# Kernel tuning notes

Hardware: AMD Instinct MI355X
Metric: run time of the kernel (lower is better)

## Reference

```python
import jax, jax.numpy as jnp
import numpy as np

NC = 80
REG_MAX = 16
STRIDES = (8.0, 16.0, 32.0)
MAX_DET = 300
IOU_THR = 0.7
CONF_THR = 0.001
NCAND = 1024        # top candidates kept before greedy NMS
MAX_WH = 7680.0     # per-class offset trick (ultralytics max_wh)


def _make_anchors(shapes, strides, offset=0.5):
    pts, strs = [], []
    for (h, w), s in zip(shapes, strides):
        sx = jnp.arange(w, dtype=jnp.float32) + offset
        sy = jnp.arange(h, dtype=jnp.float32) + offset
        gy, gx = jnp.meshgrid(sy, sx, indexing='ij')
        pts.append(jnp.stack((gx, gy), -1).reshape(-1, 2))   # (h*w, 2)
        strs.append(jnp.full((h * w, 1), s, jnp.float32))
    return jnp.concatenate(pts, 0), jnp.concatenate(strs, 0)


def _decode_raw(feats):
    """feats_to_raw_yolov8: DFL decode + anchor transform -> pixel cxcywh + sigmoid cls."""
    B = feats[0].shape[0]
    no = 4 * REG_MAX + NC
    merged = jnp.concatenate([f.reshape(B, no, -1) for f in feats], axis=2)  # (B,no,A)
    dist, cls = merged[:, :4 * REG_MAX], merged[:, 4 * REG_MAX:]
    pd = dist.transpose(0, 2, 1).reshape(B, -1, 4, REG_MAX)                  # (B,A,4,reg_max)
    proj = jnp.arange(REG_MAX, dtype=merged.dtype)
    ltrb = jnp.einsum('bafr,r->baf', jax.nn.softmax(pd, -1), proj)           # (B,A,4)
    anchors, strd = _make_anchors([f.shape[2:] for f in feats], STRIDES)     # (A,2),(A,1)
    lt, rb = ltrb[..., :2], ltrb[..., 2:]
    x1y1 = anchors[None] - lt
    x2y2 = anchors[None] + rb
    cxy = (x1y1 + x2y2) * 0.5
    wh = x2y2 - x1y1
    dbox = jnp.concatenate((cxy, wh), -1) * strd[None]                       # (B,A,4) pixel cxcywh
    return dbox, jax.nn.sigmoid(cls).transpose(0, 2, 1)                      # (B,A,nc)


def _iou_one_vs_many(box, boxes):
    lt = jnp.maximum(box[:2], boxes[:, :2])
    rb = jnp.minimum(box[2:], boxes[:, 2:])
    inter = jnp.prod(jnp.clip(rb - lt, 0.0), -1)
    a1 = jnp.prod(box[2:] - box[:2])
    a2 = jnp.prod(boxes[:, 2:] - boxes[:, :2], -1)
    return inter / (a1 + a2 - inter + 1e-7)


def _nms_image(boxes_cxcywh, scores_cls):
    """conf threshold + per-class greedy NMS + max_det truncation -> (max_det, 6)."""
    conf = scores_cls.max(-1)                                   # (A,)
    cls = jnp.argmax(scores_cls, -1).astype(jnp.float32)        # (A,)
    conf = jnp.where(conf > CONF_THR, conf, 0.0)
    top_conf, idx = jax.lax.top_k(conf, NCAND)                  # candidate pre-selection
    cb = boxes_cxcywh[idx]                                      # (NCAND,4) cxcywh
    ccls = cls[idx]
    xy1 = cb[:, :2] - cb[:, 2:] * 0.5
    xy2 = cb[:, :2] + cb[:, 2:] * 0.5
    bx = jnp.concatenate((xy1, xy2), -1) + (ccls * MAX_WH)[:, None]  # class-offset xyxy

    def step(sc, _):
        j = jnp.argmax(sc)
        s = sc[j]
        sup = _iou_one_vs_many(bx[j], bx) > IOU_THR  # self-IoU=1 kills j as well
        return jnp.where(sup, 0.0, sc), (j, s)

    _, (sel, ss) = jax.lax.scan(step, top_conf, None, length=MAX_DET)
    rows = jnp.concatenate((cb[sel], ss[:, None], ccls[sel][:, None]), -1)  # (max_det,6)
    return jnp.where((ss > CONF_THR)[:, None], rows, 0.0)


def setup_inputs() -> dict:
    key = jax.random.key(0)
    k0, k1, k2 = jax.random.split(key, 3)
    B, no = 32, 4 * REG_MAX + NC
    return {
        'feat0': jax.random.normal(k0, (B, no, 80, 80), jnp.float32),
        'feat1': jax.random.normal(k1, (B, no, 40, 40), jnp.float32),
        'feat2': jax.random.normal(k2, (B, no, 20, 20), jnp.float32),
    }


def reference(feat0, feat1, feat2):
    dbox, ps = _decode_raw([feat0, feat1, feat2])        # (B,A,4), (B,A,nc)
    return jax.vmap(_nms_image)(dbox, ps)                # (B, max_det, 6)
```

## Files before the change

kernel.cpp:

```cpp
#include <hip/hip_runtime.h>
#include <stdint.h>

#define NCLS    80
#define NA_TOT  8400
#define NBATCH  32
#define MAXDET  300
#define SSORT   2048
#define RANKCAP 1536
#define CONFTHR 0.001f
#define TILES_PER_IMG 132

__device__ __forceinline__ float xla_expf(float in) {
  const float exp_hi = 88.3762626647950f;
  const float exp_lo = -88.3762626647949f;
  const float LOG2EF = 1.44269504088896341f;
  const float C1 = 0.693359375f;
  const float C2 = -2.12194440e-4f;
  const float p0 = 1.9875691500E-4f, p1 = 1.3981999507E-3f, p2 = 8.3334519073E-3f;
  const float p3 = 4.1665795894E-2f, p4 = 1.6666665459E-1f, p5 = 5.0000001201E-1f;
  float x = fminf(fmaxf(in, exp_lo), exp_hi);
  float fx = floorf(__fadd_rn(__fmul_rn(x, LOG2EF), 0.5f));
  float tmp = __fmul_rn(C1, fx);
  float z   = __fmul_rn(C2, fx);
  x = __fsub_rn(x, tmp);
  x = __fsub_rn(x, z);
  float y = __fadd_rn(__fmul_rn(x, p0), p1);
  y = __fadd_rn(__fmul_rn(y, x), p2);
  y = __fadd_rn(__fmul_rn(y, x), p3);
  y = __fadd_rn(__fmul_rn(y, x), p4);
  y = __fadd_rn(__fmul_rn(y, x), p5);
  y = __fadd_rn(__fmul_rn(y, __fmul_rn(x, x)), x);
  y = __fadd_rn(1.0f, y);
  int m = (int)fx;
  float s = __uint_as_float((uint32_t)(m + 127) << 23);
  float r = __fmul_rn(y, s);
  return fmaxf(r, in);
}

__device__ __forceinline__ float xla_sigmoid(float v) {
  float e = xla_expf(-v);
  float den = __fadd_rn(1.0f, e);
  return 1.0f / den;
}

__device__ __forceinline__ void gload_lds16(const float* gp, float* lp) {
  __builtin_amdgcn_global_load_lds(
      (const __attribute__((address_space(1))) void*)gp,
      (__attribute__((address_space(3))) void*)lp, 16, 0, 0);
}

__global__ __launch_bounds__(256) void yolo_decode_kernel(
    const float* __restrict__ f0, const float* __restrict__ f1,
    const float* __restrict__ f2,
    float4* __restrict__ oboxes, float* __restrict__ oconf,
    float* __restrict__ oclsf) {
  __shared__ float sm[4 * 144 * 16];
  int bx  = blockIdx.x;
  int b   = bx / TILES_PER_IMG;
  int r   = bx - b * TILES_PER_IMG;
  int tid = threadIdx.x;
  int lane = tid & 63;
  int wv   = tid >> 6;

  const float* base; int Alvl, W, a0, lvlbase; float stridef;
  if (r < 100)      { base = f0 + (size_t)b * (144 * 6400); W = 80; Alvl = 6400;
                      a0 = r * 64; stridef = 8.0f; lvlbase = 0; }
  else if (r < 125) { base = f1 + (size_t)b * (144 * 1600); W = 40; Alvl = 1600;
                      a0 = (r - 100) * 64; stridef = 16.0f; lvlbase = 6400; }
  else              { base = f2 + (size_t)b * (144 * 400);  W = 20; Alvl = 400;
                      int aa = (r - 125) * 64; a0 = (aa + 64 <= 400) ? aa : 336;
                      stridef = 32.0f; lvlbase = 8000; }

  int a0w = a0 + wv * 16;
  float* Sw = sm + wv * (144 * 16);

  #pragma unroll
  for (int k = 0; k < 9; ++k) {
    int ch = k * 16 + (lane >> 2);
    const float* gp = base + (size_t)ch * Alvl + a0w + (lane & 3) * 4;
    gload_lds16(gp, Sw + k * 256);
  }
  asm volatile("s_waitcnt vmcnt(0)" ::: "memory");
  __builtin_amdgcn_sched_barrier(0);

  int idx = lane & 15;
  int w   = lane >> 4;
  int ai  = a0w + idx;
  float ax = __fadd_rn((float)(ai % W), 0.5f);
  float ay = __fadd_rn((float)(ai / W), 0.5f);

  float d[16];
  float mx = -INFINITY;
  #pragma unroll
  for (int rr = 0; rr < 16; ++rr) {
    d[rr] = Sw[(w * 16 + rr) * 16 + idx];
    mx = fmaxf(mx, d[rr]);
  }
  float e[16]; float ssum = 0.0f;
  #pragma unroll
  for (int rr = 0; rr < 16; ++rr) {
    e[rr] = xla_expf(__fsub_rn(d[rr], mx));
    ssum = __fadd_rn(ssum, e[rr]);
  }
  float acc = 0.0f;
  #pragma unroll
  for (int rr = 0; rr < 16; ++rr) {
    float p = e[rr] / ssum;
    acc = __fadd_rn(acc, __fmul_rn(p, (float)rr));
  }

  float lt0 = __shfl(acc, idx + 0);
  float lt1 = __shfl(acc, idx + 16);
  float lt2 = __shfl(acc, idx + 32);
  float lt3 = __shfl(acc, idx + 48);

  float best = -INFINITY, second = -INFINITY; int bi = 0;
  #pragma unroll 5
  for (int kk = 0; kk < 20; ++kk) {
    int c = 64 + w * 20 + kk;
    float v = Sw[c * 16 + idx];
    if (v > best)        { second = best; best = v; bi = w * 20 + kk; }
    else if (v > second) { second = v; }
  }
  float gb = __shfl(best, idx + 0), gs = __shfl(second, idx + 0);
  int   gi = __shfl(bi,   idx + 0);
  #pragma unroll
  for (int qq = 1; qq < 4; ++qq) {
    float bq = __shfl(best, idx + qq * 16), sq = __shfl(second, idx + qq * 16);
    int   iq = __shfl(bi,   idx + qq * 16);
    if (bq > gb) { gs = fmaxf(gb, sq); gb = bq; gi = iq; }
    else         { gs = fmaxf(gs, bq); }
  }

  float conf = 0.0f; int cls = gi;
  if (__fsub_rn(gb, gs) < 1e-4f || gb > 5.0f) {
    if (w == 0) {
      float bs = -INFINITY; int bj = 0;
      for (int kk = 0; kk < NCLS; ++kk) {
        float v = Sw[(64 + kk) * 16 + idx];
        float s2 = xla_sigmoid(v);
        if (s2 > bs) { bs = s2; bj = kk; }
      }
      conf = bs; cls = bj;
    }
  } else {
    conf = xla_sigmoid(gb);
  }

  if (w == 0) {
    float x1 = __fsub_rn(ax, lt0);
    float y1 = __fsub_rn(ay, lt1);
    float x2 = __fadd_rn(ax, lt2);
    float y2 = __fadd_rn(ay, lt3);
    float cx = __fmul_rn(__fadd_rn(x1, x2), 0.5f);
    float cy = __fmul_rn(__fadd_rn(y1, y2), 0.5f);
    float ww = __fsub_rn(x2, x1);
    float hh = __fsub_rn(y2, y1);
    int t = b * NA_TOT + lvlbase + a0w + idx;
    oboxes[t] = make_float4(__fmul_rn(cx, stridef), __fmul_rn(cy, stridef),
                            __fmul_rn(ww, stridef), __fmul_rn(hh, stridef));
    conf = (conf > CONFTHR) ? conf : 0.0f;
    oconf[t] = conf;
    oclsf[t] = (float)cls;
  }
}

struct __align__(16) K2Lds {
  unsigned long long sortkeys[SSORT];
  unsigned confL[NA_TOT];
  unsigned hist[16][257];
  unsigned tot[257];
  unsigned Tarr[257];
};

__global__ __launch_bounds__(1024) void yolo_select_kernel(
    const float4* __restrict__ boxes, const float* __restrict__ conf,
    const float* __restrict__ clsf,
    float* __restrict__ g_rowd, unsigned long long* __restrict__ g_clsMask) {
  __shared__ K2Lds u;
  __shared__ unsigned s_need, s_prefix, s_found, s_B, s_scnt, s_cut, s_done;
  int b    = blockIdx.x;
  int tid  = threadIdx.x;
  int lane = tid & 63;
  int wv   = tid >> 6;
  const unsigned* confu = (const unsigned*)conf + (size_t)b * NA_TOT;
  float* rowd = g_rowd + (size_t)b * 1024 * 8;
  unsigned long long* cm = g_clsMask + (size_t)b * (NCLS * 16);

  for (int i = tid; i < NA_TOT; i += 1024) u.confL[i] = confu[i];
  {
    float4 z4 = make_float4(0.f, 0.f, 0.f, 0.f);
    float4* gr = (float4*)rowd;
    for (int k = tid; k < 2048; k += 1024) gr[k] = z4;
  }
  for (int i = tid; i < NCLS * 16; i += 1024) cm[i] = 0ull;
  if (tid == 0) { s_need = 1024; s_prefix = 0; s_cut = 0; s_done = 0; s_scnt = 0; }
  __syncthreads();

  for (int lv = 0; lv < 4; ++lv) {
    __syncthreads();
    if (s_done) break;
    for (int i = tid; i < 16 * 257; i += 1024) ((unsigned*)u.hist)[i] = 0;
    if (tid == 0) { s_found = 0; s_B = 0; }
    __syncthreads();
    unsigned pfx = s_prefix;
    for (int it = 0; it < 9; ++it) {
      int i = tid + it * 1024;
      unsigned c = (i < NA_TOT) ? u.confL[i] : 0u;
      bool in; unsigned bin;
      if (lv == 0)      { in = true;                bin = c >> 23; }
      else if (lv == 1) { in = ((c >> 23) == pfx);  bin = (c >> 15) & 0xFF; }
      else if (lv == 2) { in = ((c >> 15) == pfx);  bin = (c >> 7) & 0xFF; }
      else              { in = ((c >> 7)  == pfx);  bin = c & 0x7F; }
      bool act = (c != 0) && in;
      unsigned long long ab = __ballot(act);
      if (ab) {
        int fl = __ffsll(ab) - 1;
        unsigned fbin = __shfl(bin, fl);
        unsigned long long same = __ballot(act && (bin == fbin));
        if (same == ab) {
          if (lane == fl) atomicAdd(&u.hist[wv][fbin], (unsigned)__popcll(ab));
        } else if (act) {
          atomicAdd(&u.hist[wv][bin], 1u);
        }
      }
    }
    __syncthreads();
    if (tid < 256) {
      unsigned s = 0;
      #pragma unroll
      for (int q = 0; q < 16; ++q) s += u.hist[q][tid];
      u.tot[tid] = s;
    }
    __syncthreads();
    if (tid < 64) {
      unsigned carry = 0;
      if (tid == 0) u.Tarr[256] = 0;
      for (int ch = 3; ch >= 0; --ch) {
        int bb = ch * 64 + tid;
        unsigned v = u.tot[bb];
        #pragma unroll
        for (int off = 1; off < 64; off <<= 1) {
          unsigned t2 = __shfl_down(v, off);
          if (tid + off < 64) v += t2;
        }
        u.Tarr[bb] = v + carry;
        carry += __shfl(v, 0);
      }
    }
    __syncthreads();
    unsigned need = s_need;
    if (tid < 256) {
      unsigned h = u.tot[tid];
      if (h > 0 && u.Tarr[tid + 1] < need && u.Tarr[tid + 1] + h >= need) {
        s_B = (unsigned)tid; s_found = 1;
      }
    }
    __syncthreads();
    if (tid == 0) {
      if (!s_found) { s_cut = 1; s_done = 1; }
      else {
        unsigned B = s_B;
        unsigned selcnt = (1024u - need) + u.Tarr[B];
        if (selcnt <= (unsigned)RANKCAP || lv == 3) {
          s_done = 1;
          if (lv == 0)      s_cut = B << 23;
          else if (lv == 1) s_cut = (s_prefix << 23) | (B << 15);
          else if (lv == 2) s_cut = (s_prefix << 15) | (B << 7);
          else              s_cut = (s_prefix << 7)  | B;
        } else {
          s_need   = need - u.Tarr[B + 1];
          s_prefix = (s_prefix << 8) | B;
        }
      }
    }
  }
  __syncthreads();

  unsigned cut = s_cut;
  for (int it = 0; it < 9; ++it) {
    int i = tid + it * 1024;
    unsigned c = (i < NA_TOT) ? u.confL[i] : 0u;
    bool sel = (c != 0 && c >= cut);
    unsigned long long bal = __ballot(sel);
    unsigned base2 = 0;
    if (lane == 0 && bal) base2 = atomicAdd(&s_scnt, (unsigned)__popcll(bal));
    base2 = __shfl(base2, 0);
    if (sel) {
      unsigned p = base2 + (unsigned)__popcll(bal & ((1ull << lane) - 1ull));
      if (p < SSORT)
        u.sortkeys[p] = ((unsigned long long)c << 32) |
                        (unsigned long long)(0xFFFFFFFFu - (unsigned)i);
    }
  }
  __syncthreads();
  unsigned scnt = s_scnt; if (scnt > SSORT) scnt = SSORT;
  unsigned snp = (scnt + 1u) & ~1u;
  if (tid == 0 && (scnt & 1u)) u.sortkeys[scnt] = 0ull;
  __syncthreads();

  for (unsigned e = tid; e < scnt; e += 1024) {
    unsigned long long mykey = u.sortkeys[e];
    unsigned r = 0;
    #pragma unroll 4
    for (unsigned j = 0; j < snp; j += 2) {
      ulonglong2 kk = *reinterpret_cast<const ulonglong2*>(&u.sortkeys[j]);
      r += (kk.x > mykey) ? 1u : 0u;
      r += (kk.y > mykey) ? 1u : 0u;
    }
    if (r < 1024) {
      unsigned a = 0xFFFFFFFFu - (unsigned)(mykey & 0xFFFFFFFFull);
      float4 cb = boxes[(size_t)b * NA_TOT + a];
      float cls = clsf[(size_t)b * NA_TOT + a];
      float4* gr = (float4*)(rowd + (size_t)r * 8);
      gr[0] = cb;
      gr[1] = make_float4(__uint_as_float((unsigned)(mykey >> 32)), cls, 0.f, 0.f);
      atomicOr(&cm[(int)cls * 16 + (r >> 6)], 1ull << (r & 63));
    }
  }
}

struct K3Lds {
  unsigned long long rows[1024][16];
  float    rowdata[1024][6];
  unsigned long long am[16];
};

__global__ __launch_bounds__(1024) void yolo_nms_kernel(
    const float* __restrict__ g_rowd,
    const unsigned long long* __restrict__ g_clsMask,
    float* __restrict__ out) {
  __shared__ K3Lds u;
  __shared__ unsigned s_sticky, s_fill;
  int b    = blockIdx.x;
  int tid  = threadIdx.x;
  const unsigned long long* cm = g_clsMask + (size_t)b * (NCLS * 16);

  {
    const float4* gr = (const float4*)(g_rowd + ((size_t)b * 1024 + tid) * 8);
    float4 v0 = gr[0];
    float4 v1 = gr[1];
    u.rowdata[tid][0] = v0.x; u.rowdata[tid][1] = v0.y;
    u.rowdata[tid][2] = v0.z; u.rowdata[tid][3] = v0.w;
    u.rowdata[tid][4] = v1.x; u.rowdata[tid][5] = v1.y;
  }
  {
    unsigned long long* flat = &u.rows[0][0];
    for (int k = tid; k < 1024 * 16; k += 1024) flat[k] = 0ull;
  }
  if (tid < 16) u.am[tid] = 0ull;
  if (tid == 0) { s_sticky = 0xFFFFFFFFu; s_fill = 0; }
  __syncthreads();

  {
    float cls = u.rowdata[tid][5];
    int c = (int)cls;
    const unsigned long long* cmask = cm + c * 16;
    bool valid = (cmask[tid >> 6] >> (tid & 63)) & 1ull;
    if (valid) {
      float bx0 = u.rowdata[tid][0], by0 = u.rowdata[tid][1];
      float bw0 = u.rowdata[tid][2], bh0 = u.rowdata[tid][3];
      float off = __fmul_rn(cls, 7680.0f);
      float hw  = __fmul_rn(bw0, 0.5f), hh = __fmul_rn(bh0, 0.5f);
      float wx1 = __fadd_rn(__fsub_rn(bx0, hw), off);
      float wy1 = __fadd_rn(__fsub_rn(by0, hh), off);
      float wx2 = __fadd_rn(__fadd_rn(bx0, hw), off);
      float wy2 = __fadd_rn(__fadd_rn(by0, hh), off);
      float a1  = __fmul_rn(__fsub_rn(wx2, wx1), __fsub_rn(wy2, wy1));
      int sw = tid & 15;
      for (int q = 0; q < 16; ++q) {
        unsigned long long m = cmask[q];
        while (m) {
          int bit = __ffsll(m) - 1;
          m &= m - 1ull;
          int j = q * 64 + bit;
          float jx = u.rowdata[j][0], jy = u.rowdata[j][1];
          float jw = u.rowdata[j][2], jh = u.rowdata[j][3];
          float jhw = __fmul_rn(jw, 0.5f), jhh = __fmul_rn(jh, 0.5f);
          float jx1 = __fadd_rn(__fsub_rn(jx, jhw), off);
          float jy1 = __fadd_rn(__fsub_rn(jy, jhh), off);
          float jx2 = __fadd_rn(__fadd_rn(jx, jhw), off);
          float jy2 = __fadd_rn(__fadd_rn(jy, jhh), off);
          float ltx = fmaxf(wx1, jx1), lty = fmaxf(wy1, jy1);
          float rbx = fminf(wx2, jx2), rby = fminf(wy2, jy2);
          float iw = fmaxf(__fsub_rn(rbx, ltx), 0.0f);
          float ih = fmaxf(__fsub_rn(rby, lty), 0.0f);
          float inter = __fmul_rn(iw, ih);
          float a2 = __fmul_rn(__fsub_rn(jx2, jx1), __fsub_rn(jy2, jy1));
          float den = __fadd_rn(__fsub_rn(__fadd_rn(a1, a2), inter), 1e-7f);
          float iou = inter / den;
          if (iou > 0.7f)
            u.rows[tid][(j >> 6) ^ sw] |= (1ull << (j & 63));
        }
      }
    }
  }
  __syncthreads();

  if (tid < NCLS) {
    const unsigned long long* cmask = cm + tid * 16;
    unsigned long long alive[16];
    bool any = false;
    #pragma unroll
    for (int q = 0; q < 16; ++q) { alive[q] = cmask[q]; any |= (alive[q] != 0ull); }
    while (any) {
      int r = -1;
      #pragma unroll
      for (int q = 0; q < 16; ++q)
        if (r < 0 && alive[q]) r = q * 64 + (__ffsll(alive[q]) - 1);
      atomicOr(&u.am[r >> 6], 1ull << (r & 63));
      int sw = r & 15;
      unsigned long long selfw = u.rows[r][(r >> 6) ^ sw];
      bool selfbit = (selfw >> (r & 63)) & 1ull;
      if (!selfbit) { atomicMin(&s_sticky, (unsigned)r); break; }
      any = false;
      #pragma unroll
      for (int q = 0; q < 16; ++q) {
        alive[q] &= ~u.rows[r][q ^ sw];
        any |= (alive[q] != 0ull);
      }
    }
  }
  __syncthreads();

  unsigned rs = s_sticky;
  {
    unsigned r = (unsigned)tid;
    bool surv = (u.am[r >> 6] >> (r & 63)) & 1ull;
    if (surv && r <= rs) {
      unsigned e2 = 0;
      int hi = (int)(r >> 6);
      #pragma unroll
      for (int q = 0; q < 16; ++q) {
        unsigned long long m = u.am[q];
        if (q < hi)       e2 += (unsigned)__popcll(m);
        else if (q == hi) e2 += (unsigned)__popcll(m & ((1ull << (r & 63)) - 1ull));
      }
      if (e2 < MAXDET) {
        float* orow = out + (size_t)b * (MAXDET * 6) + (size_t)e2 * 6;
        orow[0] = u.rowdata[r][0];
        orow[1] = u.rowdata[r][1];
        orow[2] = u.rowdata[r][2];
        orow[3] = u.rowdata[r][3];
        orow[4] = u.rowdata[r][4];
        orow[5] = u.rowdata[r][5];
      }
    }
  }
  if (tid == 0) {
    unsigned fill;
    if (rs != 0xFFFFFFFFu) {
      unsigned es = 0;
      int hi = (int)(rs >> 6);
      #pragma unroll
      for (int q = 0; q < 16; ++q) {
        unsigned long long m = u.am[q];
        if (q < hi)       es += (unsigned)__popcll(m);
        else if (q == hi) es += (unsigned)__popcll(m & ((1ull << (rs & 63)) - 1ull));
      }
      fill = es + 1;
    } else {
      unsigned S = 0;
      #pragma unroll
      for (int q = 0; q < 16; ++q) S += (unsigned)__popcll(u.am[q]);
      fill = S;
    }
    s_fill = (fill > (unsigned)MAXDET) ? (unsigned)MAXDET : fill;
  }
  __syncthreads();

  {
    unsigned fill = s_fill;
    bool st = (rs != 0xFFFFFFFFu);
    float* orow = out + (size_t)b * (MAXDET * 6);
    for (int i = (int)fill * 6 + tid; i < MAXDET * 6; i += 1024) {
      float v = 0.0f;
      if (st) v = u.rowdata[rs][i - (i / 6) * 6];
      orow[i] = v;
    }
  }
}

extern "C" void kernel_launch(void* const* d_in, const int* in_sizes, int n_in,
                              void* d_out, int out_size, void* d_ws, size_t ws_size,
                              hipStream_t stream) {
  const float* f0 = (const float*)d_in[0];
  const float* f1 = (const float*)d_in[1];
  const float* f2 = (const float*)d_in[2];
  float* out = (float*)d_out;

  char* ws = (char*)d_ws;
  float4* boxes = (float4*)ws;
  float*  conf  = (float*)(ws + (size_t)NBATCH * NA_TOT * 16);
  float*  clsf  = (float*)(ws + (size_t)NBATCH * NA_TOT * 20);
  float*  rowd  = (float*)(ws + (size_t)NBATCH * NA_TOT * 24);
  unsigned long long* clsm =
      (unsigned long long*)(ws + (size_t)NBATCH * NA_TOT * 24 + 1048576);

  yolo_decode_kernel<<<NBATCH * TILES_PER_IMG, 256, 0, stream>>>(
      f0, f1, f2, boxes, conf, clsf);
  yolo_select_kernel<<<NBATCH, 1024, 0, stream>>>(boxes, conf, clsf, rowd, clsm);
  yolo_nms_kernel<<<NBATCH, 1024, 0, stream>>>(rowd, clsm, out);
}
```

Baseline: 135.7 us.

## Split candidate rank-sort into a separate wider-grid kernel

The O(n^2) rank computation over the selected candidate keys moves out of the per-image select kernel (32 blocks of 1024 threads) into a new kernel with 8 blocks of 256 threads per image. Each new block reloads the image's keys from global memory into LDS and ranks its own slice. The aim is to spread the quadratic comparison work across more compute units, since 32 blocks leave most of the GPU idle. The cost is an extra kernel launch plus a global round trip for the keys and count.

```diff
diff --git a/kernel.cpp b/kernel.cpp
--- a/kernel.cpp
+++ b/kernel.cpp
@@ -9,6 +9,7 @@
 #define RANKCAP 1536
 #define CONFTHR 0.001f
 #define TILES_PER_IMG 132
+#define GKCAP   2056
 
 __device__ __forceinline__ float xla_expf(float in) {
   const float exp_hi = 88.3762626647950f;
@@ -166,7 +167,6 @@
 }
 
 struct __align__(16) K2Lds {
-  unsigned long long sortkeys[SSORT];
   unsigned confL[NA_TOT];
   unsigned hist[16][257];
   unsigned tot[257];
@@ -174,8 +174,8 @@
 };
 
 __global__ __launch_bounds__(1024) void yolo_select_kernel(
-    const float4* __restrict__ boxes, const float* __restrict__ conf,
-    const float* __restrict__ clsf,
+    const float* __restrict__ conf,
+    unsigned long long* __restrict__ g_keys, unsigned* __restrict__ g_scnt,
     float* __restrict__ g_rowd, unsigned long long* __restrict__ g_clsMask) {
   __shared__ K2Lds u;
   __shared__ unsigned s_need, s_prefix, s_found, s_B, s_scnt, s_cut, s_done;
@@ -184,16 +184,16 @@
   int lane = tid & 63;
   int wv   = tid >> 6;
   const unsigned* confu = (const unsigned*)conf + (size_t)b * NA_TOT;
-  float* rowd = g_rowd + (size_t)b * 1024 * 8;
-  unsigned long long* cm = g_clsMask + (size_t)b * (NCLS * 16);
+  unsigned long long* gk = g_keys + (size_t)b * GKCAP;
 
   for (int i = tid; i < NA_TOT; i += 1024) u.confL[i] = confu[i];
   {
     float4 z4 = make_float4(0.f, 0.f, 0.f, 0.f);
-    float4* gr = (float4*)rowd;
+    float4* gr = (float4*)(g_rowd + (size_t)b * 1024 * 8);
     for (int k = tid; k < 2048; k += 1024) gr[k] = z4;
   }
-  for (int i = tid; i < NCLS * 16; i += 1024) cm[i] = 0ull;
+  for (int i = tid; i < NCLS * 16; i += 1024)
+    g_clsMask[(size_t)b * (NCLS * 16) + i] = 0ull;
   if (tid == 0) { s_need = 1024; s_prefix = 0; s_cut = 0; s_done = 0; s_scnt = 0; }
   __syncthreads();
 
@@ -289,34 +289,56 @@
     if (sel) {
       unsigned p = base2 + (unsigned)__popcll(bal & ((1ull << lane) - 1ull));
       if (p < SSORT)
-        u.sortkeys[p] = ((unsigned long long)c << 32) |
-                        (unsigned long long)(0xFFFFFFFFu - (unsigned)i);
-    }
-  }
-  __syncthreads();
-  unsigned scnt = s_scnt; if (scnt > SSORT) scnt = SSORT;
-  unsigned snp = (scnt + 1u) & ~1u;
-  if (tid == 0 && (scnt & 1u)) u.sortkeys[scnt] = 0ull;
-  __syncthreads();
-
-  for (unsigned e = tid; e < scnt; e += 1024) {
-    unsigned long long mykey = u.sortkeys[e];
-    unsigned r = 0;
-    #pragma unroll 4
-    for (unsigned j = 0; j < snp; j += 2) {
-      ulonglong2 kk = *reinterpret_cast<const ulonglong2*>(&u.sortkeys[j]);
-      r += (kk.x > mykey) ? 1u : 0u;
-      r += (kk.y > mykey) ? 1u : 0u;
-    }
-    if (r < 1024) {
-      unsigned a = 0xFFFFFFFFu - (unsigned)(mykey & 0xFFFFFFFFull);
-      float4 cb = boxes[(size_t)b * NA_TOT + a];
-      float cls = clsf[(size_t)b * NA_TOT + a];
-      float4* gr = (float4*)(rowd + (size_t)r * 8);
-      gr[0] = cb;
-      gr[1] = make_float4(__uint_as_float((unsigned)(mykey >> 32)), cls, 0.f, 0.f);
-      atomicOr(&cm[(int)cls * 16 + (r >> 6)], 1ull << (r & 63));
-    }
+        gk[p] = ((unsigned long long)c << 32) |
+                (unsigned long long)(0xFFFFFFFFu - (unsigned)i);
+    }
+  }
+  __syncthreads();
+  if (tid == 0) {
+    unsigned sc = s_scnt; if (sc > SSORT) sc = SSORT;
+    g_scnt[b] = sc;
+    if (sc & 1u) gk[sc] = 0ull;
+  }
+}
+
+__global__ __launch_bounds__(256) void yolo_rank_kernel(
+    const unsigned long long* __restrict__ g_keys,
+    const unsigned* __restrict__ g_scnt,
+    const float4* __restrict__ boxes, const float* __restrict__ clsf,
+    float* __restrict__ g_rowd, unsigned long long* __restrict__ g_clsMask) {
+  __shared__ __align__(16) unsigned long long lk[GKCAP];
+  int bx   = blockIdx.x;
+  int b    = bx >> 3;
+  int part = bx & 7;
+  int tid  = threadIdx.x;
+  const unsigned long long* gk = g_keys + (size_t)b * GKCAP;
+  unsigned scnt = g_scnt[b];
+  unsigned snp  = (scnt + 1u) & ~1u;
+
+  for (unsigned i = tid; i < snp; i += 256) lk[i] = gk[i];
+  __syncthreads();
+
+  unsigned e = (unsigned)(part * 256 + tid);
+  if (e >= scnt) return;
+  unsigned long long mykey = lk[e];
+  unsigned r = 0;
+  #pragma unroll 4
+  for (unsigned j = 0; j < snp; j += 2) {
+    ulonglong2 kk = *reinterpret_cast<const ulonglong2*>(&lk[j]);
+    r += (kk.x > mykey) ? 1u : 0u;
+    r += (kk.y > mykey) ? 1u : 0u;
+  }
+
+  if (r < 1024) {
+    unsigned a = 0xFFFFFFFFu - (unsigned)(mykey & 0xFFFFFFFFull);
+    float4 cb = boxes[(size_t)b * NA_TOT + a];
+    float cls = clsf[(size_t)b * NA_TOT + a];
+    float* rowd = g_rowd + (size_t)b * 1024 * 8;
+    float4* gr = (float4*)(rowd + (size_t)r * 8);
+    gr[0] = cb;
+    gr[1] = make_float4(__uint_as_float((unsigned)(mykey >> 32)), cls, 0.f, 0.f);
+    atomicOr(&g_clsMask[(size_t)b * (NCLS * 16) + (int)cls * 16 + (r >> 6)],
+             1ull << (r & 63));
   }
 }
 
@@ -493,12 +515,17 @@
   float4* boxes = (float4*)ws;
   float*  conf  = (float*)(ws + (size_t)NBATCH * NA_TOT * 16);
   float*  clsf  = (float*)(ws + (size_t)NBATCH * NA_TOT * 20);
-  float*  rowd  = (float*)(ws + (size_t)NBATCH * NA_TOT * 24);
-  unsigned long long* clsm =
-      (unsigned long long*)(ws + (size_t)NBATCH * NA_TOT * 24 + 1048576);
+  size_t off = (size_t)NBATCH * NA_TOT * 24;
+  float*  rowd  = (float*)(ws + off);                         off += 1048576;
+  unsigned long long* clsm  = (unsigned long long*)(ws + off); off += 327680;
+  unsigned long long* gkeys = (unsigned long long*)(ws + off); off += (size_t)NBATCH * GKCAP * 8;
+  unsigned* scnts = (unsigned*)(ws + off);
 
   yolo_decode_kernel<<<NBATCH * TILES_PER_IMG, 256, 0, stream>>>(
       f0, f1, f2, boxes, conf, clsf);
-  yolo_select_kernel<<<NBATCH, 1024, 0, stream>>>(boxes, conf, clsf, rowd, clsm);
+  yolo_select_kernel<<<NBATCH, 1024, 0, stream>>>(conf, gkeys, scnts,
+                                                  rowd, clsm);
+  yolo_rank_kernel<<<NBATCH * 8, 256, 0, stream>>>(gkeys, scnts, boxes, clsf,
+                                                   rowd, clsm);
   yolo_nms_kernel<<<NBATCH, 1024, 0, stream>>>(rowd, clsm, out);
 }
```

Result: faster. 123.8 us, median of 2 (-8.8%).
